# Kernel tuning notes

Measured on AMD Instinct MI355X. Metric: run time of the kernel, lower is better.

Reference implementation:

```python
import jax, jax.numpy as jnp
import numpy as np


def _gcn_conv(x, edge_index, W, b):
    """PyG GCNConv: add self-loops, symmetric normalization, scatter-add aggregation."""
    N = x.shape[0]
    loops = jnp.arange(N, dtype=edge_index.dtype)
    src = jnp.concatenate([edge_index[0], loops])  # [E+N]
    dst = jnp.concatenate([edge_index[1], loops])  # [E+N]
    # degree computed on destination nodes (flow: source_to_target)
    deg = jax.ops.segment_sum(jnp.ones_like(dst, dtype=x.dtype), dst, num_segments=N)
    deg_inv_sqrt = jnp.where(deg > 0, jax.lax.rsqrt(jnp.maximum(deg, 1.0)), 0.0)
    norm = deg_inv_sqrt[src] * deg_inv_sqrt[dst]  # [E+N]
    h = x @ W  # [N, out]
    msg = h[src] * norm[:, None]  # [E+N, out]
    out = jax.ops.segment_sum(msg, dst, num_segments=N)
    return out + b


def setup_inputs() -> dict:
    key = jax.random.key(0)
    k1, k2, k3, k4 = jax.random.split(key, 4)
    N, E, D_IN, D_HID, D_OUT = 100000, 1600000, 128, 128, 64
    x = jax.random.normal(k1, (N, D_IN), dtype=jnp.float32)
    edge_index = jax.random.randint(k2, (2, E), 0, N, dtype=jnp.int64)
    batch = jnp.zeros((N,), dtype=jnp.int64)
    W1 = jax.random.normal(k3, (D_IN, D_HID), dtype=jnp.float32) / np.sqrt(D_IN)
    b1 = jnp.zeros((D_HID,), dtype=jnp.float32)
    W2 = jax.random.normal(k4, (D_HID, D_OUT), dtype=jnp.float32) / np.sqrt(D_HID)
    b2 = jnp.zeros((D_OUT,), dtype=jnp.float32)
    return {"x": x, "edge_index": edge_index, "batch": batch,
            "W1": W1, "b1": b1, "W2": W2, "b2": b2}


def reference(x, edge_index, batch, W1, b1, W2, b2):
    h = _gcn_conv(x, edge_index, W1, b1)
    h = jax.nn.relu(h)
    # dropout is identity at inference (training=False)
    out = _gcn_conv(h, edge_index, W2, b2)
    # original computes F.log_softmax but discards it; returns out
    return out
```

## Files before the change

### kernel.cpp

```cpp
#include <hip/hip_runtime.h>
#include <hip/hip_fp16.h>


#define KDIM 128
#define BSHIFT 9
#define BSIZE 512
#define ECHUNK 2048
#define CAP 10240
#define PACK_SHIFT 20
#define PACK_MASK ((1u << PACK_SHIFT) - 1)

typedef _Float16 h8 __attribute__((ext_vector_type(8)));
typedef float f4v __attribute__((ext_vector_type(4)));


__launch_bounds__(256) __global__
void bscatter_kernel(const int* __restrict__ src, const int* __restrict__ dst,
                     int* __restrict__ ecnt, unsigned int* __restrict__ packed_out,
                     int E, int NB) {
    __shared__ int lcnt[256];
    __shared__ int lexc[256];
    __shared__ int lbase[256];
    __shared__ unsigned int lpacked[ECHUNK];
    __shared__ unsigned char lbslot[ECHUNK];

    const int t = threadIdx.x;
    lcnt[t] = 0;
    __syncthreads();

    const int base = blockIdx.x * ECHUNK;
    const int cnt = min(ECHUNK, E - base);

#pragma unroll
    for (int j = 0; j < ECHUNK / 256; j++) {
        int e = base + j * 256 + t;
        if (e < E) atomicAdd(&lcnt[dst[e] >> BSHIFT], 1);
    }
    __syncthreads();

    lexc[t] = lcnt[t];
    __syncthreads();
    for (int off = 1; off < 256; off <<= 1) {
        int x = (t >= off) ? lexc[t - off] : 0;
        __syncthreads();
        if (t >= off) lexc[t] += x;
        __syncthreads();
    }
    lexc[t] = lexc[t] - lcnt[t];

    if (t < NB && lcnt[t]) lbase[t] = t * CAP + atomicAdd(&ecnt[t], lcnt[t]);
    __syncthreads();
    lcnt[t] = lexc[t];
    __syncthreads();

#pragma unroll
    for (int j = 0; j < ECHUNK / 256; j++) {
        int e = base + j * 256 + t;
        if (e < E) {
            int d = dst[e];
            int b = d >> BSHIFT;
            int pos = atomicAdd(&lcnt[b], 1);
            lpacked[pos] = (unsigned int)src[e] | ((unsigned int)(d & (BSIZE - 1)) << PACK_SHIFT);
            lbslot[pos] = (unsigned char)b;
        }
    }
    __syncthreads();

#pragma unroll
    for (int j = 0; j < ECHUNK / 256; j++) {
        int s = j * 256 + t;
        if (s < cnt) {
            int b = lbslot[s];
            int pos = lbase[b] + (s - lexc[b]);
            if (pos < (b + 1) * CAP)
                packed_out[pos] = lpacked[s];
        }
    }
}


__launch_bounds__(1024) __global__
void bfinal_kernel(const unsigned int* __restrict__ packed, const int* __restrict__ ecnt,
                   int* __restrict__ rowptr, float* __restrict__ dinv,
                   int* __restrict__ ssrc, int N, int E, int NB) {
    __shared__ int ncnt[BSIZE];
    __shared__ int sbuf[BSIZE];
    __shared__ int bsc[256];
    __shared__ int bbase_sh;

    const int t = threadIdx.x;
    const int b = blockIdx.x;

    if (t < 256) bsc[t] = (t < NB) ? min(ecnt[t], CAP) : 0;
    if (t < BSIZE) ncnt[t] = 0;
    __syncthreads();

    const int cnt = min(ecnt[b], CAP);
    const unsigned int* pb = packed + (size_t)b * CAP;
    unsigned int held[CAP / 1024];
#pragma unroll
    for (int j = 0; j < CAP / 1024; j++) {
        int e = t + j * 1024;
        if (e < cnt) {
            unsigned int p = pb[e];
            held[j] = p;
            atomicAdd(&ncnt[p >> PACK_SHIFT], 1);
        }
    }

    __syncthreads();
    for (int off = 1; off < 256; off <<= 1) {
        int x = 0;
        if (t < 256 && t >= off) x = bsc[t - off];
        __syncthreads();
        if (t < 256 && t >= off) bsc[t] += x;
        __syncthreads();
    }
    if (t == 0) bbase_sh = (b == 0) ? 0 : bsc[b - 1];

    int mycnt = 0;
    if (t < BSIZE) {
        mycnt = ncnt[t];
        sbuf[t] = mycnt;
    }
    __syncthreads();
    for (int off = 1; off < BSIZE; off <<= 1) {
        int x = 0;
        if (t < BSIZE && t >= off) x = sbuf[t - off];
        __syncthreads();
        if (t < BSIZE && t >= off) sbuf[t] += x;
        __syncthreads();
    }

    const int gb = bbase_sh;
    if (t < BSIZE) {
        int exc = (t == 0) ? 0 : sbuf[t - 1];
        int node = (b << BSHIFT) + t;
        if (node < N) {
            rowptr[node] = gb + exc;
            dinv[node] = rsqrtf((float)(mycnt + 1));
        }
        ncnt[t] = gb + exc;
    }
    if (t == 0 && b == NB - 1) rowptr[N] = gb + cnt;
    __syncthreads();

#pragma unroll
    for (int j = 0; j < CAP / 1024; j++) {
        int e = t + j * 1024;
        if (e < cnt) {
            unsigned int p = held[j];
            int d = p >> PACK_SHIFT;
            int pos = atomicAdd(&ncnt[d], 1);
            ssrc[pos] = (int)(p & PACK_MASK);
        }
    }
}


__device__ inline h8 pack8(float4 u, float4 v) {
    h8 r;
    r[0] = (_Float16)u.x; r[1] = (_Float16)u.y; r[2] = (_Float16)u.z; r[3] = (_Float16)u.w;
    r[4] = (_Float16)v.x; r[5] = (_Float16)v.y; r[6] = (_Float16)v.z; r[7] = (_Float16)v.w;
    return r;
}

template <int DOUT, bool AHALF>
__launch_bounds__(256) __global__
void gemm_mfma_kernel(const void* __restrict__ Xv, const float* __restrict__ W,
                      const float* __restrict__ dinv, _Float16* __restrict__ outh, int N) {
    constexpr int K = KDIM;
    constexpr int KS = K + 8;
    constexpr int NT = DOUT / 16;
    __shared__ _Float16 Wl[DOUT * KS];

    const int t = threadIdx.x;
    const int wave = t >> 6;
    const int lane = t & 63;
    const int l15 = lane & 15;
    const int quad = lane >> 4;

#pragma unroll
    for (int i = t; i < DOUT * (K / 4); i += 256) {
        int n = i & (DOUT - 1);
        int kg = i / DOUT;
        union { _Float16 h[4]; uint2 u; } tmp;
#pragma unroll
        for (int j = 0; j < 4; j++)
            tmp.h[j] = (_Float16)W[(size_t)(kg * 4 + j) * DOUT + n];
        *(uint2*)(&Wl[n * KS + kg * 4]) = tmp.u;
    }
    __syncthreads();

    const int rowbase = blockIdx.x * 128;
    const int row0 = rowbase + wave * 32 + l15;
    const int row1 = row0 + 16;
    const int rc0 = min(row0, N - 1);
    const int rc1 = min(row1, N - 1);

    f4v acc[2][NT];
#pragma unroll
    for (int r = 0; r < 2; r++)
#pragma unroll
        for (int ct = 0; ct < NT; ct++) acc[r][ct] = (f4v)0.0f;

#pragma unroll
    for (int kc = 0; kc < K; kc += 32) {
        const int kof = kc + quad * 8;
        h8 a0, a1;
        if (AHALF) {
            const _Float16* Xh = (const _Float16*)Xv;
            a0 = *(const h8*)(Xh + (size_t)rc0 * K + kof);
            a1 = *(const h8*)(Xh + (size_t)rc1 * K + kof);
        } else {
            const float* Xf = (const float*)Xv;
            const float* p0 = Xf + (size_t)rc0 * K + kof;
            const float* p1 = Xf + (size_t)rc1 * K + kof;
            a0 = pack8(*(const float4*)p0, *(const float4*)(p0 + 4));
            a1 = pack8(*(const float4*)p1, *(const float4*)(p1 + 4));
        }
#pragma unroll
        for (int ct = 0; ct < NT; ct++) {
            h8 b = *(const h8*)(&Wl[(size_t)(ct * 16 + l15) * KS + kof]);
            acc[0][ct] = __builtin_amdgcn_mfma_f32_16x16x32_f16(a0, b, acc[0][ct], 0, 0, 0);
            acc[1][ct] = __builtin_amdgcn_mfma_f32_16x16x32_f16(a1, b, acc[1][ct], 0, 0, 0);
        }
    }

#pragma unroll
    for (int r = 0; r < 2; r++) {
        const int rb = rowbase + wave * 32 + r * 16 + quad * 4;
#pragma unroll
        for (int g = 0; g < 4; g++) {
            int row = rb + g;
            if (row < N) {
                float di = dinv[row];
                _Float16* op = outh + (size_t)row * DOUT + l15;
#pragma unroll
                for (int ct = 0; ct < NT; ct++)
                    op[ct * 16] = (_Float16)(acc[r][ct][g] * di);
            }
        }
    }
}


template <int DOUT, bool RELU, bool HOUT>
__launch_bounds__(256) __global__
void agg_kernel(const __half* __restrict__ hs, const int* __restrict__ rowptr,
                const int* __restrict__ ssrc, const float* __restrict__ dinv,
                const float* __restrict__ bias, void* __restrict__ outv, int N) {
    constexpr int TPN = DOUT / 8;
    const int npb = blockDim.x / TPN;
    const int node = blockIdx.x * npb + threadIdx.x / TPN;
    if (node >= N) return;
    const int lane = threadIdx.x % TPN;
    const int c0 = lane * 8;

    float acc[8];
    {
        uint4 u = *(const uint4*)(hs + (size_t)node * DOUT + c0);
        const __half2* hp = (const __half2*)&u;
#pragma unroll
        for (int q = 0; q < 4; q++) {
            float2 f = __half22float2(hp[q]);
            acc[2 * q] = f.x;
            acc[2 * q + 1] = f.y;
        }
    }

    const int e0 = rowptr[node];
    const int e1 = rowptr[node + 1];
    int e = e0;
    for (; e + 4 <= e1; e += 4) {
        int s0 = ssrc[e + 0];
        int s1 = ssrc[e + 1];
        int s2 = ssrc[e + 2];
        int s3 = ssrc[e + 3];
        uint4 u0 = *(const uint4*)(hs + (size_t)s0 * DOUT + c0);
        uint4 u1 = *(const uint4*)(hs + (size_t)s1 * DOUT + c0);
        uint4 u2 = *(const uint4*)(hs + (size_t)s2 * DOUT + c0);
        uint4 u3 = *(const uint4*)(hs + (size_t)s3 * DOUT + c0);
        const __half2* p0 = (const __half2*)&u0;
        const __half2* p1 = (const __half2*)&u1;
        const __half2* p2 = (const __half2*)&u2;
        const __half2* p3 = (const __half2*)&u3;
#pragma unroll
        for (int q = 0; q < 4; q++) {
            float2 f0 = __half22float2(p0[q]);
            float2 f1 = __half22float2(p1[q]);
            float2 f2 = __half22float2(p2[q]);
            float2 f3 = __half22float2(p3[q]);
            acc[2 * q]     += (f0.x + f1.x) + (f2.x + f3.x);
            acc[2 * q + 1] += (f0.y + f1.y) + (f2.y + f3.y);
        }
    }
    for (; e < e1; e++) {
        int s = ssrc[e];
        uint4 u = *(const uint4*)(hs + (size_t)s * DOUT + c0);
        const __half2* hp = (const __half2*)&u;
#pragma unroll
        for (int q = 0; q < 4; q++) {
            float2 f = __half22float2(hp[q]);
            acc[2 * q] += f.x;
            acc[2 * q + 1] += f.y;
        }
    }

    const float di = dinv[node];
    float o[8];
#pragma unroll
    for (int q = 0; q < 2; q++) {
        float4 bq = *(const float4*)(bias + c0 + 4 * q);
        o[4 * q + 0] = di * acc[4 * q + 0] + bq.x;
        o[4 * q + 1] = di * acc[4 * q + 1] + bq.y;
        o[4 * q + 2] = di * acc[4 * q + 2] + bq.z;
        o[4 * q + 3] = di * acc[4 * q + 3] + bq.w;
    }
    if (RELU) {
#pragma unroll
        for (int j = 0; j < 8; j++) o[j] = fmaxf(o[j], 0.f);
    }
    if (HOUT) {
        union { __half2 h[4]; uint4 u; } pk;
#pragma unroll
        for (int q = 0; q < 4; q++)
            pk.h[q] = __floats2half2_rn(o[2 * q], o[2 * q + 1]);
        *(uint4*)((__half*)outv + (size_t)node * DOUT + c0) = pk.u;
    } else {
        float* op = (float*)outv + (size_t)node * DOUT + c0;
        *(float4*)op = make_float4(o[0], o[1], o[2], o[3]);
        *(float4*)(op + 4) = make_float4(o[4], o[5], o[6], o[7]);
    }
}


extern "C" void kernel_launch(void* const* d_in, const int* in_sizes, int n_in,
                              void* d_out, int out_size, void* d_ws, size_t ws_size,
                              hipStream_t stream) {
    const float* x  = (const float*)d_in[0];
    const int*   ei = (const int*)d_in[1];
    const float* W1 = (const float*)d_in[3];
    const float* b1 = (const float*)d_in[4];
    const float* W2 = (const float*)d_in[5];
    const float* b2 = (const float*)d_in[6];
    float* out = (float*)d_out;

    const int N = in_sizes[0] / KDIM;
    const int E = in_sizes[1] / 2;
    const int* esrc = ei;
    const int* edst = ei + E;
    const int NB = (N + BSIZE - 1) >> BSHIFT;

    char* ws = (char*)d_ws;
    size_t off = 0;
    auto alloc = [&](size_t bytes) {
        size_t p = off;
        off = (off + bytes + 511) & ~(size_t)511;
        return p;
    };
    int*      ecnt    = (int*)(ws + alloc((size_t)NB * 4));
    int*      rowptr  = (int*)(ws + alloc((size_t)(N + 1) * 4));
    float*    dinv    = (float*)(ws + alloc((size_t)N * 4));
    int*      ssrc    = (int*)(ws + alloc((size_t)E * 4));
    _Float16* hs      = (_Float16*)(ws + alloc((size_t)N * KDIM * 2));
    _Float16* out1    = (_Float16*)(ws + alloc((size_t)N * KDIM * 2));
    unsigned int* packed = (unsigned int*)hs;
    (void)ws_size; (void)n_in; (void)out_size;

    const int eb = (E + ECHUNK - 1) / ECHUNK;

    hipMemsetAsync(ecnt, 0, (size_t)NB * 4, stream);

    bscatter_kernel<<<eb, 256, 0, stream>>>(esrc, edst, ecnt, packed, E, NB);
    bfinal_kernel<<<NB, 1024, 0, stream>>>(packed, ecnt, rowptr, dinv, ssrc, N, E, NB);

    gemm_mfma_kernel<128, false><<<(N + 127) / 128, 256, 0, stream>>>(x, W1, dinv, hs, N);
    agg_kernel<128, true, true><<<(N + 15) / 16, 256, 0, stream>>>(
        (const __half*)hs, rowptr, ssrc, dinv, b1, out1, N);

    gemm_mfma_kernel<64, true><<<(N + 127) / 128, 256, 0, stream>>>(out1, W2, dinv, hs, N);
    agg_kernel<64, false, false><<<(N + 31) / 32, 256, 0, stream>>>(
        (const __half*)hs, rowptr, ssrc, dinv, b2, out, N);
}
```

Measured before the change: 264.0 us.

## Fuse layer-1 aggregation with layer-2 GEMM via LDS and MFMA

Adds a kernel that aggregates neighbor features for 16 nodes per block, applies bias and ReLU, stages the fp16 result in LDS, and multiplies it by W2 with MFMA before writing the layer-2 pre-scaled features. This removes the separate layer-2 GEMM launch and the global round trip of the intermediate activation. In exchange, every block reloads and converts W2 from fp32 into LDS, which adds per-block overhead and LDS pressure that may reduce occupancy.

Result: no change. 261.5 us (-1.0%).

```diff
diff --git a/kernel.cpp b/kernel.cpp
--- a/kernel.cpp
+++ b/kernel.cpp
@@ -241,6 +241,131 @@
                     op[ct * 16] = (_Float16)(acc[r][ct][g] * di);
             }
         }
+    }
+}
+
+
+__launch_bounds__(256) __global__
+void agg_gemm_kernel(const __half* __restrict__ hs, const int* __restrict__ rowptr,
+                     const int* __restrict__ ssrc, const float* __restrict__ dinv,
+                     const float* __restrict__ bias, const float* __restrict__ W2,
+                     _Float16* __restrict__ hs2, int N) {
+    constexpr int K = KDIM;
+    constexpr int KS = K + 8;
+    constexpr int DO2 = 64;
+    __shared__ _Float16 W2l[DO2 * KS];
+    __shared__ _Float16 o_lds[16 * KS];
+
+    const int t = threadIdx.x;
+
+#pragma unroll
+    for (int i = t; i < DO2 * (K / 4); i += 256) {
+        int n = i & (DO2 - 1);
+        int kg = i / DO2;
+        union { _Float16 h[4]; uint2 u; } tmp;
+#pragma unroll
+        for (int j = 0; j < 4; j++)
+            tmp.h[j] = (_Float16)W2[(size_t)(kg * 4 + j) * DO2 + n];
+        *(uint2*)(&W2l[n * KS + kg * 4]) = tmp.u;
+    }
+
+    const int nl = t >> 4;
+    const int node = blockIdx.x * 16 + nl;
+    const int flane = t & 15;
+    const int c0 = flane * 8;
+
+    h8 oh;
+    if (node < N) {
+        float acc[8];
+        {
+            uint4 u = *(const uint4*)(hs + (size_t)node * K + c0);
+            const __half2* hp = (const __half2*)&u;
+#pragma unroll
+            for (int q = 0; q < 4; q++) {
+                float2 f = __half22float2(hp[q]);
+                acc[2 * q] = f.x;
+                acc[2 * q + 1] = f.y;
+            }
+        }
+
+        const int e0 = rowptr[node];
+        const int e1 = rowptr[node + 1];
+        int e = e0;
+        for (; e + 4 <= e1; e += 4) {
+            int s0 = ssrc[e + 0];
+            int s1 = ssrc[e + 1];
+            int s2 = ssrc[e + 2];
+            int s3 = ssrc[e + 3];
+            uint4 u0 = *(const uint4*)(hs + (size_t)s0 * K + c0);
+            uint4 u1 = *(const uint4*)(hs + (size_t)s1 * K + c0);
+            uint4 u2 = *(const uint4*)(hs + (size_t)s2 * K + c0);
+            uint4 u3 = *(const uint4*)(hs + (size_t)s3 * K + c0);
+            const __half2* p0 = (const __half2*)&u0;
+            const __half2* p1 = (const __half2*)&u1;
+            const __half2* p2 = (const __half2*)&u2;
+            const __half2* p3 = (const __half2*)&u3;
+#pragma unroll
+            for (int q = 0; q < 4; q++) {
+                float2 f0 = __half22float2(p0[q]);
+                float2 f1 = __half22float2(p1[q]);
+                float2 f2 = __half22float2(p2[q]);
+                float2 f3 = __half22float2(p3[q]);
+                acc[2 * q]     += (f0.x + f1.x) + (f2.x + f3.x);
+                acc[2 * q + 1] += (f0.y + f1.y) + (f2.y + f3.y);
+            }
+        }
+        for (; e < e1; e++) {
+            int s = ssrc[e];
+            uint4 u = *(const uint4*)(hs + (size_t)s * K + c0);
+            const __half2* hp = (const __half2*)&u;
+#pragma unroll
+            for (int q = 0; q < 4; q++) {
+                float2 f = __half22float2(hp[q]);
+                acc[2 * q] += f.x;
+                acc[2 * q + 1] += f.y;
+            }
+        }
+
+        const float di = dinv[node];
+#pragma unroll
+        for (int q = 0; q < 2; q++) {
+            float4 bq = *(const float4*)(bias + c0 + 4 * q);
+            float o0 = fmaxf(di * acc[4 * q + 0] + bq.x, 0.f);
+            float o1 = fmaxf(di * acc[4 * q + 1] + bq.y, 0.f);
+            float o2 = fmaxf(di * acc[4 * q + 2] + bq.z, 0.f);
+            float o3 = fmaxf(di * acc[4 * q + 3] + bq.w, 0.f);
+            oh[4 * q + 0] = (_Float16)o0;
+            oh[4 * q + 1] = (_Float16)o1;
+            oh[4 * q + 2] = (_Float16)o2;
+            oh[4 * q + 3] = (_Float16)o3;
+        }
+    } else {
+#pragma unroll
+        for (int j = 0; j < 8; j++) oh[j] = (_Float16)0.f;
+    }
+
+    *(h8*)(&o_lds[nl * KS + c0]) = oh;
+    __syncthreads();
+
+    const int wv = t >> 6;
+    const int l15 = t & 15;
+    const int quad = (t & 63) >> 4;
+
+    f4v a2 = (f4v)0.0f;
+#pragma unroll
+    for (int kc = 0; kc < K; kc += 32) {
+        const int kof = kc + quad * 8;
+        h8 a = *(const h8*)(&o_lds[l15 * KS + kof]);
+        h8 b = *(const h8*)(&W2l[(size_t)(wv * 16 + l15) * KS + kof]);
+        a2 = __builtin_amdgcn_mfma_f32_16x16x32_f16(a, b, a2, 0, 0, 0);
+    }
+
+    const int rowbase = blockIdx.x * 16;
+#pragma unroll
+    for (int g = 0; g < 4; g++) {
+        int r = rowbase + quad * 4 + g;
+        if (r < N)
+            hs2[(size_t)r * DO2 + wv * 16 + l15] = (_Float16)(a2[g] * dinv[r]);
     }
 }
 
@@ -363,9 +488,9 @@
     int*      rowptr  = (int*)(ws + alloc((size_t)(N + 1) * 4));
     float*    dinv    = (float*)(ws + alloc((size_t)N * 4));
     int*      ssrc    = (int*)(ws + alloc((size_t)E * 4));
-    _Float16* hs      = (_Float16*)(ws + alloc((size_t)N * KDIM * 2));
-    _Float16* out1    = (_Float16*)(ws + alloc((size_t)N * KDIM * 2));
-    unsigned int* packed = (unsigned int*)hs;
+    _Float16* hs1     = (_Float16*)(ws + alloc((size_t)N * KDIM * 2));
+    _Float16* hs2     = (_Float16*)(ws + alloc((size_t)N * 64 * 2));
+    unsigned int* packed = (unsigned int*)hs1;
     (void)ws_size; (void)n_in; (void)out_size;
 
     const int eb = (E + ECHUNK - 1) / ECHUNK;
@@ -375,11 +500,11 @@
     bscatter_kernel<<<eb, 256, 0, stream>>>(esrc, edst, ecnt, packed, E, NB);
     bfinal_kernel<<<NB, 1024, 0, stream>>>(packed, ecnt, rowptr, dinv, ssrc, N, E, NB);
 
-    gemm_mfma_kernel<128, false><<<(N + 127) / 128, 256, 0, stream>>>(x, W1, dinv, hs, N);
-    agg_kernel<128, true, true><<<(N + 15) / 16, 256, 0, stream>>>(
-        (const __half*)hs, rowptr, ssrc, dinv, b1, out1, N);
-
-    gemm_mfma_kernel<64, true><<<(N + 127) / 128, 256, 0, stream>>>(out1, W2, dinv, hs, N);
+    gemm_mfma_kernel<128, false><<<(N + 127) / 128, 256, 0, stream>>>(x, W1, dinv, hs1, N);
+
+    agg_gemm_kernel<<<(N + 15) / 16, 256, 0, stream>>>(
+        (const __half*)hs1, rowptr, ssrc, dinv, b1, W2, hs2, N);
+
     agg_kernel<64, false, false><<<(N + 31) / 32, 256, 0, stream>>>(
-        (const __half*)hs, rowptr, ssrc, dinv, b2, out, N);
-}
+        (const __half*)hs2, rowptr, ssrc, dinv, b2, out, N);
+}
```
